# Optimization experiments

Hardware: AMD Instinct MI355X
Metric: run time of the kernel (lower is better)

The kernel has to match this reference:

```python
import jax, jax.numpy as jnp
import numpy as np

N_NODES = 131072   # total nodes across all ego-graphs
B = 16384          # number of graphs (ego nodes)
N_PER = N_NODES // B  # nodes per graph (uniform for the synthetic batch)
IN_CH = 1024
OUT_CH = 512
NUM_CENTERS = 16


def setup_inputs() -> dict:
    key = jax.random.key(0)
    k1, k2, k3, k4 = jax.random.split(key, 4)
    gnn_x = jax.random.normal(k1, (N_NODES, IN_CH), dtype=jnp.float32)
    Wc = jax.random.normal(k2, (NUM_CENTERS, IN_CH), dtype=jnp.float32) * (IN_CH ** -0.5)
    W_experts = jax.random.normal(k3, (NUM_CENTERS, OUT_CH, IN_CH), dtype=jnp.float32) * (IN_CH ** -0.5)
    # sorted segment ids: graph g owns nodes [g*N_PER, (g+1)*N_PER)
    batch = (jnp.arange(N_NODES) // N_PER).astype(jnp.int64)
    # ego node offset within each graph
    ego_idx = jax.random.randint(k4, (B,), 0, N_PER).astype(jnp.int64)
    return {"gnn_x": gnn_x, "Wc": Wc, "W_experts": W_experts, "batch": batch, "ego_idx": ego_idx}


def reference(gnn_x, Wc, W_experts, batch, ego_idx):
    # get_ds_x: first node index of each graph (diff_idxs) + per-graph ego offset
    n_graphs = ego_idx.shape[0]
    starts = jnp.searchsorted(batch, jnp.arange(n_graphs, dtype=batch.dtype))  # [B]
    ego_idxs = starts + ego_idx                                               # [B]
    ds_x = gnn_x[ego_idxs]                                                    # [B, in]

    # route each ego embedding to one of num_centers experts via argmax
    center_scores = ds_x @ Wc.T                 # [B, num_centers]
    center_idx = jnp.argmax(center_scores, axis=1)  # [B]

    # per-node expert linear: logits[b] = W_experts[center_idx[b]] @ ds_x[b]
    W_sel = W_experts[center_idx]               # [B, out, in]
    logits = jnp.einsum('bi,boi->bo', ds_x, W_sel)  # [B, out]
    return logits
```

## Files before the change

### kernel.cpp

```cpp
#include <hip/hip_runtime.h>
#include <hip/hip_bf16.h>
#include <stdint.h>

#define N_NODES_C 131072
#define B_C       16384
#define IN_C      1024
#define OUT_C     512
#define NC_C      16

typedef short s16x8 __attribute__((ext_vector_type(8)));
typedef float f32x4 __attribute__((ext_vector_type(4)));

__device__ __forceinline__ unsigned short f2bf(float f) {
  union { float f; unsigned u; } v; v.f = f;
  unsigned u = v.u;
  unsigned r = (u + 0x7fffu + ((u >> 16) & 1u)) >> 16;
  return (unsigned short)r;
}

__device__ __forceinline__ void async_cp16(void* lds, const void* g) {
  __builtin_amdgcn_global_load_lds(
      (const __attribute__((address_space(1))) unsigned int*)g,
      (__attribute__((address_space(3))) unsigned int*)lds, 16, 0, 0);
}

__global__ __launch_bounds__(512) void k_fused(
    const float* __restrict__ W, unsigned short* __restrict__ Wb,
    const float* __restrict__ gnn_x, const float* __restrict__ Wc,
    const int* __restrict__ batch, const int* __restrict__ ego_idx,
    unsigned short* __restrict__ xb, int* __restrict__ rows_sorted,
    int* __restrict__ cursors) {
  const int bid = blockIdx.x;
  const int t = threadIdx.x;

  if (bid >= 512) {
    const int i = ((bid - 512) * 512 + t) * 4;
    float4 v = *(const float4*)&W[i];
    ushort4 h;
    h.x = f2bf(v.x); h.y = f2bf(v.y); h.z = f2bf(v.z); h.w = f2bf(v.w);
    *(ushort4*)&Wb[i] = h;
    return;
  }

  __shared__ float wc[NC_C * IN_C];
  __shared__ int sbest[32];
  __shared__ int sbase[16];

  for (int i = t * 4; i < NC_C * IN_C; i += 512 * 4)
    *(float4*)&wc[i] = *(const float4*)&Wc[i];
  __syncthreads();

  const int w = t >> 6, l = t & 63;
  const int gbase = bid * 32;
  const int gw = gbase + w * 4;

  const int gq = gw + (l & 3);
  int lo = 0, hi = N_NODES_C;
  while (lo < hi) { int mid = (lo + hi) >> 1; if (batch[mid] < gq) lo = mid + 1; else hi = mid; }
  const int srcq = lo + ego_idx[gq];

  #pragma unroll
  for (int rr = 0; rr < 4; ++rr) {
    const int g = gw + rr;
    const int src_row = __shfl(srcq, rr, 64);
    const float* xp = gnn_x + (size_t)src_row * IN_C;

    float4 xv[4];
    #pragma unroll
    for (int j = 0; j < 4; ++j) xv[j] = *(const float4*)&xp[j * 256 + l * 4];

    unsigned short* dst = &xb[(size_t)g * IN_C];
    #pragma unroll
    for (int j = 0; j < 4; ++j) {
      ushort4 h;
      h.x = f2bf(xv[j].x); h.y = f2bf(xv[j].y); h.z = f2bf(xv[j].z); h.w = f2bf(xv[j].w);
      *(ushort4*)&dst[j * 256 + l * 4] = h;
    }

    float sc[NC_C];
    #pragma unroll
    for (int c = 0; c < NC_C; ++c) {
      float a = 0.f;
      #pragma unroll
      for (int j = 0; j < 4; ++j) {
        float4 wv = *(const float4*)&wc[c * IN_C + j * 256 + l * 4];
        a += xv[j].x * wv.x + xv[j].y * wv.y + xv[j].z * wv.z + xv[j].w * wv.w;
      }
      #pragma unroll
      for (int off = 32; off > 0; off >>= 1) a += __shfl_xor(a, off, 64);
      sc[c] = a;
    }
    if (l == 0) {
      int best = 0; float bv = sc[0];
      #pragma unroll
      for (int c = 1; c < NC_C; ++c) if (sc[c] > bv) { bv = sc[c]; best = c; }
      sbest[w * 4 + rr] = best;
    }
  }

  __syncthreads();
  if (t < 16) {
    int n = 0;
    #pragma unroll
    for (int r = 0; r < 32; ++r) n += (sbest[r] == t);
    if (n) sbase[t] = atomicAdd(&cursors[t * 16], n);
  }
  __syncthreads();
  if (t < 32) {
    const int c = sbest[t];
    int rank = 0;
    for (int r = 0; r < t; ++r) rank += (sbest[r] == c);
    rows_sorted[c * B_C + sbase[c] + rank] = gbase + t;
  }
}

__global__ __launch_bounds__(512) void k_gemm(
    const unsigned short* __restrict__ xb, const unsigned short* __restrict__ Wb,
    const int* __restrict__ rows_sorted, const int* __restrict__ cnts,
    float* __restrict__ out) {
  const int i = blockIdx.x + 4 * blockIdx.y + 512 * blockIdx.z;
  const int xcd = i & 7;
  const int j = i >> 3;
  const int e = xcd * 2 + (j & 1);
  const int r = j >> 1;
  const int mt = r >> 2;
  const int nt = r & 3;

  const int cnt = cnts[e * 16];
  const int m0 = mt * 128;
  if (m0 >= cnt) return;
  const int n0 = nt * 128;

  __shared__ unsigned short Al[2][128 * 64];
  __shared__ unsigned short Bl[2][128 * 64];

  const int t = threadIdx.x;
  const int w = t >> 6, l = t & 63;

  const int srow = t >> 3;
  const int scolb = (t & 7) * 16;
  const char* bbase = (const char*)Wb + ((size_t)e * OUT_C + n0) * (IN_C * 2);
  const char* aptr[2];
  const char* bptr[2];
  #pragma unroll
  for (int ii = 0; ii < 2; ++ii) {
    const int row = srow + ii * 64;
    const int sw = scolb ^ ((row & 7) << 4);
    const int p = m0 + row;
    const int rid = (p < cnt) ? rows_sorted[e * B_C + p] : 0;
    aptr[ii] = (const char*)xb + (size_t)rid * (IN_C * 2) + sw;
    bptr[ii] = bbase + (size_t)row * (IN_C * 2) + sw;
  }

  const f32x4 fz = {0.f, 0.f, 0.f, 0.f};
  f32x4 acc[2][4];
  #pragma unroll
  for (int mi = 0; mi < 2; ++mi)
    #pragma unroll
    for (int ni = 0; ni < 4; ++ni) acc[mi][ni] = fz;

#define STAGE(buf, kt) do {                                        \
    char* ab_ = (char*)&Al[buf][0] + w * 1024;                     \
    char* bb_ = (char*)&Bl[buf][0] + w * 1024;                     \
    const size_t ko_ = (size_t)(kt) * 128;                         \
    _Pragma("unroll")                                              \
    for (int i_ = 0; i_ < 2; ++i_) {                               \
      async_cp16(ab_ + i_ * 8192, aptr[i_] + ko_);                 \
      async_cp16(bb_ + i_ * 8192, bptr[i_] + ko_);                 \
    }                                                              \
  } while (0)

  STAGE(0, 0);
  __syncthreads();

  const int wm = w >> 1, wn = w & 1;
  const int lrow = l & 15, kg = l >> 4;
  const int NKT = IN_C / 64;

  int cur = 0;
  for (int kt = 0; kt < NKT; ++kt) {
    if (kt + 1 < NKT) STAGE(cur ^ 1, kt + 1);
    #pragma unroll
    for (int ks = 0; ks < 2; ++ks) {
      const int cb = ks * 64 + kg * 16;
      s16x8 a[2], b[4];
      #pragma unroll
      for (int mi = 0; mi < 2; ++mi) {
        const int row = wm * 32 + mi * 16 + lrow;
        a[mi] = *(const s16x8*)((const char*)&Al[cur][0] + row * 128 + (cb ^ ((row & 7) << 4)));
      }
      #pragma unroll
      for (int ni = 0; ni < 4; ++ni) {
        const int row = wn * 64 + ni * 16 + lrow;
        b[ni] = *(const s16x8*)((const char*)&Bl[cur][0] + row * 128 + (cb ^ ((row & 7) << 4)));
      }
      #pragma unroll
      for (int mi = 0; mi < 2; ++mi)
        #pragma unroll
        for (int ni = 0; ni < 4; ++ni)
          acc[mi][ni] = __builtin_amdgcn_mfma_f32_16x16x32_bf16(a[mi], b[ni], acc[mi][ni], 0, 0, 0);
    }
    __syncthreads();
    cur ^= 1;
  }
#undef STAGE

  #pragma unroll
  for (int mi = 0; mi < 2; ++mi) {
    #pragma unroll
    for (int reg = 0; reg < 4; ++reg) {
      const int p = m0 + wm * 32 + mi * 16 + kg * 4 + reg;
      if (p < cnt) {
        const int rid = rows_sorted[e * B_C + p];
        float* orow = out + (size_t)rid * OUT_C + n0 + wn * 64 + lrow;
        #pragma unroll
        for (int ni = 0; ni < 4; ++ni) orow[ni * 16] = acc[mi][ni][reg];
      }
    }
  }
}

extern "C" void kernel_launch(void* const* d_in, const int* in_sizes, int n_in,
                              void* d_out, int out_size, void* d_ws, size_t ws_size,
                              hipStream_t stream) {
  const float* gnn_x     = (const float*)d_in[0];
  const float* Wc        = (const float*)d_in[1];
  const float* W_experts = (const float*)d_in[2];
  const int*   batch     = (const int*)d_in[3];
  const int*   ego_idx   = (const int*)d_in[4];
  float* out = (float*)d_out;

  uint8_t* ws = (uint8_t*)d_ws;
  unsigned short* xb     = (unsigned short*)ws;
  unsigned short* W_bf16 = (unsigned short*)(ws + 33554432);
  int* rows_sorted = (int*)(ws + 50331648);
  int* cursors     = (int*)(ws + 51380224);

  hipMemsetAsync(cursors, 0, NC_C * 16 * sizeof(int), stream);
  k_fused<<<dim3(512 + 4096), dim3(512), 0, stream>>>(W_experts, W_bf16, gnn_x, Wc,
                                                      batch, ego_idx, xb, rows_sorted, cursors);
  k_gemm<<<dim3(OUT_C / 128, B_C / 128, NC_C), dim3(512), 0, stream>>>(xb, W_bf16, rows_sorted, cursors, out);
}
```

Baseline: 88.64 us.

## Deepen GEMM LDS pipeline to four stages with K=32 tiles and explicit vmcnt waits

The expert GEMM's double-buffered K=64 LDS staging becomes a 4-slot ring of K=32 tiles, with three tiles prefetched ahead. Explicit s_waitcnt vmcnt counts and raw s_barrier replace the __syncthreads so that only the current tile's loads are waited on. The swizzle is redone for 64-byte rows. The aim is to hide global-load latency better. In exchange there are twice as many barrier rounds per K, less MFMA work between barriers, and correctness now depends on hand-counted vmcnt values.

New measurement: 92.43 us. +4.3%, slower.

```diff
diff --git a/kernel.cpp b/kernel.cpp
--- a/kernel.cpp
+++ b/kernel.cpp
@@ -131,26 +131,19 @@
   if (m0 >= cnt) return;
   const int n0 = nt * 128;
 
-  __shared__ unsigned short Al[2][128 * 64];
-  __shared__ unsigned short Bl[2][128 * 64];
+  __shared__ unsigned short Al[4][128 * 32];
+  __shared__ unsigned short Bl[4][128 * 32];
 
   const int t = threadIdx.x;
   const int w = t >> 6, l = t & 63;
 
-  const int srow = t >> 3;
-  const int scolb = (t & 7) * 16;
-  const char* bbase = (const char*)Wb + ((size_t)e * OUT_C + n0) * (IN_C * 2);
-  const char* aptr[2];
-  const char* bptr[2];
-  #pragma unroll
-  for (int ii = 0; ii < 2; ++ii) {
-    const int row = srow + ii * 64;
-    const int sw = scolb ^ ((row & 7) << 4);
-    const int p = m0 + row;
-    const int rid = (p < cnt) ? rows_sorted[e * B_C + p] : 0;
-    aptr[ii] = (const char*)xb + (size_t)rid * (IN_C * 2) + sw;
-    bptr[ii] = bbase + (size_t)row * (IN_C * 2) + sw;
-  }
+  const int srow = t >> 2;
+  const int scolb = (t & 3) * 16;
+  const int ssw = scolb ^ (((srow >> 1) & 3) << 4);
+  const int p = m0 + srow;
+  const int rid = (p < cnt) ? rows_sorted[e * B_C + p] : 0;
+  const char* aptr = (const char*)xb + (size_t)rid * (IN_C * 2) + ssw;
+  const char* bptr = (const char*)Wb + ((size_t)e * OUT_C + n0 + srow) * (IN_C * 2) + ssw;
 
   const f32x4 fz = {0.f, 0.f, 0.f, 0.f};
   f32x4 acc[2][4];
@@ -160,48 +153,56 @@
     for (int ni = 0; ni < 4; ++ni) acc[mi][ni] = fz;
 
 #define STAGE(buf, kt) do {                                        \
-    char* ab_ = (char*)&Al[buf][0] + w * 1024;                     \
-    char* bb_ = (char*)&Bl[buf][0] + w * 1024;                     \
-    const size_t ko_ = (size_t)(kt) * 128;                         \
-    _Pragma("unroll")                                              \
-    for (int i_ = 0; i_ < 2; ++i_) {                               \
-      async_cp16(ab_ + i_ * 8192, aptr[i_] + ko_);                 \
-      async_cp16(bb_ + i_ * 8192, bptr[i_] + ko_);                 \
-    }                                                              \
+    const size_t ko_ = (size_t)(kt) * 64;                          \
+    async_cp16((char*)&Al[buf][0] + w * 1024, aptr + ko_);         \
+    async_cp16((char*)&Bl[buf][0] + w * 1024, bptr + ko_);         \
   } while (0)
 
   STAGE(0, 0);
-  __syncthreads();
+  STAGE(1, 1);
+  STAGE(2, 2);
 
   const int wm = w >> 1, wn = w & 1;
   const int lrow = l & 15, kg = l >> 4;
-  const int NKT = IN_C / 64;
-
-  int cur = 0;
+  const int cb = kg * 16;
+  const int NKT = IN_C / 32;
+
+  #pragma unroll 4
   for (int kt = 0; kt < NKT; ++kt) {
-    if (kt + 1 < NKT) STAGE(cur ^ 1, kt + 1);
-    #pragma unroll
-    for (int ks = 0; ks < 2; ++ks) {
-      const int cb = ks * 64 + kg * 16;
-      s16x8 a[2], b[4];
-      #pragma unroll
-      for (int mi = 0; mi < 2; ++mi) {
-        const int row = wm * 32 + mi * 16 + lrow;
-        a[mi] = *(const s16x8*)((const char*)&Al[cur][0] + row * 128 + (cb ^ ((row & 7) << 4)));
-      }
-      #pragma unroll
-      for (int ni = 0; ni < 4; ++ni) {
-        const int row = wn * 64 + ni * 16 + lrow;
-        b[ni] = *(const s16x8*)((const char*)&Bl[cur][0] + row * 128 + (cb ^ ((row & 7) << 4)));
-      }
-      #pragma unroll
-      for (int mi = 0; mi < 2; ++mi)
-        #pragma unroll
-        for (int ni = 0; ni < 4; ++ni)
-          acc[mi][ni] = __builtin_amdgcn_mfma_f32_16x16x32_bf16(a[mi], b[ni], acc[mi][ni], 0, 0, 0);
-    }
-    __syncthreads();
-    cur ^= 1;
+    if (kt + 3 < NKT) {
+      STAGE((kt + 3) & 3, kt + 3);
+      asm volatile("s_waitcnt vmcnt(6)" ::: "memory");
+    } else if (kt == NKT - 3) {
+      asm volatile("s_waitcnt vmcnt(4)" ::: "memory");
+    } else if (kt == NKT - 2) {
+      asm volatile("s_waitcnt vmcnt(2)" ::: "memory");
+    } else {
+      asm volatile("s_waitcnt vmcnt(0)" ::: "memory");
+    }
+    __builtin_amdgcn_s_barrier();
+    asm volatile("" ::: "memory");
+
+    const char* Ab = (const char*)&Al[kt & 3][0];
+    const char* Bb = (const char*)&Bl[kt & 3][0];
+    s16x8 a[2], b[4];
+    #pragma unroll
+    for (int mi = 0; mi < 2; ++mi) {
+      const int row = wm * 32 + mi * 16 + lrow;
+      a[mi] = *(const s16x8*)(Ab + row * 64 + (cb ^ (((row >> 1) & 3) << 4)));
+    }
+    #pragma unroll
+    for (int ni = 0; ni < 4; ++ni) {
+      const int row = wn * 64 + ni * 16 + lrow;
+      b[ni] = *(const s16x8*)(Bb + row * 64 + (cb ^ (((row >> 1) & 3) << 4)));
+    }
+    #pragma unroll
+    for (int mi = 0; mi < 2; ++mi)
+      #pragma unroll
+      for (int ni = 0; ni < 4; ++ni)
+        acc[mi][ni] = __builtin_amdgcn_mfma_f32_16x16x32_bf16(a[mi], b[ni], acc[mi][ni], 0, 0, 0);
+
+    asm volatile("" ::: "memory");
+    __builtin_amdgcn_s_barrier();
   }
 #undef STAGE
 
@@ -209,10 +210,10 @@
   for (int mi = 0; mi < 2; ++mi) {
     #pragma unroll
     for (int reg = 0; reg < 4; ++reg) {
-      const int p = m0 + wm * 32 + mi * 16 + kg * 4 + reg;
-      if (p < cnt) {
-        const int rid = rows_sorted[e * B_C + p];
-        float* orow = out + (size_t)rid * OUT_C + n0 + wn * 64 + lrow;
+      const int pp = m0 + wm * 32 + mi * 16 + kg * 4 + reg;
+      if (pp < cnt) {
+        const int orid = rows_sorted[e * B_C + pp];
+        float* orow = out + (size_t)orid * OUT_C + n0 + wn * 64 + lrow;
         #pragma unroll
         for (int ni = 0; ni < 4; ++ni) orow[ni * 16] = acc[mi][ni][reg];
       }
```
